# Performance work log

Measured on AMD Instinct MI355X. Metric: run time of the kernel, lower is better.

The kernel has to match this reference:

```python
import jax, jax.numpy as jnp
import numpy as np

B, SQ, SK, D, H = 4, 2048, 2048, 1024, 16
HD = D // H
LN_EPS = 1e-5


def setup_inputs() -> dict:
    key = jax.random.key(0)
    ks = jax.random.split(key, 16)
    s = 0.02
    return {
        "query": jax.random.normal(ks[0], (B, SQ, D), jnp.float32),
        "key": jax.random.normal(ks[1], (B, SK, D), jnp.float32),
        "value": jax.random.normal(ks[2], (B, SK, D), jnp.float32),
        "attention_mask": jax.random.randint(ks[3], (B, 1, 1, SK), 0, 2, jnp.int32),
        "relative_position_bias": jax.random.normal(ks[4], (1, H, SQ, SK), jnp.float32) * s,
        "Wq": jax.random.normal(ks[5], (D, D), jnp.float32) * s,
        "bq": jnp.zeros((D,), jnp.float32),
        "Wk": jax.random.normal(ks[6], (D, D), jnp.float32) * s,
        "bk": jnp.zeros((D,), jnp.float32),
        "Wv": jax.random.normal(ks[7], (D, D), jnp.float32) * s,
        "bv": jnp.zeros((D,), jnp.float32),
        "Wo": jax.random.normal(ks[8], (D, D), jnp.float32) * s,
        "bo": jnp.zeros((D,), jnp.float32),
        "ln_gamma": jnp.ones((D,), jnp.float32),
        "ln_beta": jnp.zeros((D,), jnp.float32),
    }


def reference(query, key, value, attention_mask, relative_position_bias,
              Wq, bq, Wk, bk, Wv, bv, Wo, bo, ln_gamma, ln_beta):
    # projections (torch Linear: x @ W.T + b)
    q = query @ Wq.T + bq   # [B,Sq,D]
    k = key @ Wk.T + bk     # [B,Sk,D]
    v = value @ Wv.T + bv   # [B,Sk,D]
    # split heads -> [B,H,S,hd]
    q = q.reshape(B, SQ, H, HD).transpose(0, 2, 1, 3)
    k = k.reshape(B, SK, H, HD).transpose(0, 2, 1, 3)
    v = v.reshape(B, SK, H, HD).transpose(0, 2, 1, 3)
    scores = jnp.einsum('bhqd,bhkd->bhqk', q, k) / jnp.sqrt(jnp.float32(HD))
    scores = scores + relative_position_bias
    scores = jnp.where(attention_mask == 0, -jnp.inf, scores)
    weights = jax.nn.softmax(scores, axis=-1)  # [B,H,Sq,Sk]
    ctx = jnp.einsum('bhqk,bhkd->bhqd', weights, v)
    ctx = ctx.transpose(0, 2, 1, 3).reshape(B, SQ, D)
    out = ctx @ Wo.T + bo
    x = query + out
    mu = jnp.mean(x, axis=-1, keepdims=True)
    var = jnp.var(x, axis=-1, keepdims=True)
    return (x - mu) * jax.lax.rsqrt(var + LN_EPS) * ln_gamma + ln_beta
```

## Files before the change

### kernel.cpp

```cpp
#include <hip/hip_runtime.h>
#include <hip/hip_bf16.h>

#define B_   4
#define SQ_  2048
#define SK_  2048
#define D_   1024
#define H_   16
#define HD_  64

typedef __bf16 bf16_t;
typedef bf16_t bf16x8 __attribute__((ext_vector_type(8)));
typedef bf16_t bf16x4 __attribute__((ext_vector_type(4)));
typedef float  f32x4  __attribute__((ext_vector_type(4)));
typedef int    i32x4  __attribute__((ext_vector_type(4)));
typedef unsigned u32x2 __attribute__((ext_vector_type(2)));



__device__ __forceinline__ void gll16(const bf16_t* g, bf16_t* l) {
    __builtin_amdgcn_global_load_lds(
        (const __attribute__((address_space(1))) unsigned int*)g,
        (__attribute__((address_space(3))) unsigned int*)l, 16, 0, 0);
}

__global__ __launch_bounds__(256) void cvt_bf16(
    const float* __restrict__ p0, const float* __restrict__ p1,
    const float* __restrict__ p2, const float* __restrict__ p3,
    bf16_t* __restrict__ d, int n)
{
    int y = blockIdx.y;
    const float* s = (y == 0) ? p0 : (y == 1) ? p1 : (y == 2) ? p2 : p3;
    int i = (blockIdx.x * 256 + threadIdx.x) * 8;
    f32x4 a = *(const f32x4*)(s + i);
    f32x4 b = *(const f32x4*)(s + i + 4);
    bf16x8 o;
    #pragma unroll
    for (int j = 0; j < 4; j++) { o[j] = (bf16_t)a[j]; o[4 + j] = (bf16_t)b[j]; }
    *(bf16x8*)(d + (size_t)y * n + i) = o;
}

__global__ __launch_bounds__(256) void gemm_qkv(
    const bf16_t* __restrict__ xb,
    const bf16_t* __restrict__ wb,
    const float* __restrict__ bq, const float* __restrict__ bk, const float* __restrict__ bv,
    bf16_t* __restrict__ oq, bf16_t* __restrict__ ok, bf16_t* __restrict__ ov)
{
    __shared__ __align__(16) bf16_t lA[2][4096];
    __shared__ __align__(16) bf16_t lB[2][4096];

    int z = blockIdx.z;
    const bf16_t* A = xb + (size_t)z * 8192 * 1024;
    const bf16_t* Bm = wb + (size_t)z * 1024 * 1024;
    const float* bias = (z == 0) ? bq : (z == 1) ? bk : bv;
    bf16_t* out = (z == 0) ? oq : (z == 1) ? ok : ov;

    int tid = threadIdx.x;
    int w = tid >> 6, l = tid & 63, lr = l & 15, lg = l >> 4;
    int m0 = blockIdx.x * 128, n0 = blockIdx.y * 128;
    int wm = (w >> 1) * 64, wn = (w & 1) * 64;

    f32x4 zero4 = {0.f, 0.f, 0.f, 0.f};
    f32x4 acc[4][4];
    #pragma unroll
    for (int i = 0; i < 4; i++)
        #pragma unroll
        for (int j = 0; j < 4; j++) acc[i][j] = zero4;

    int s0 = tid, s1 = 256 + tid;
    int r0 = s0 >> 2, c0 = s0 & 3, r1 = s1 >> 2, c1 = s1 & 3;
    const bf16_t* a0 = A + (size_t)(m0 + r0) * 1024 + ((c0 ^ ((r0 >> 1) & 3)) * 8);
    const bf16_t* a1 = A + (size_t)(m0 + r1) * 1024 + ((c1 ^ ((r1 >> 1) & 3)) * 8);
    const bf16_t* b0 = Bm + (size_t)(n0 + r0) * 1024 + ((c0 ^ ((r0 >> 1) & 3)) * 8);
    const bf16_t* b1 = Bm + (size_t)(n0 + r1) * 1024 + ((c1 ^ ((r1 >> 1) & 3)) * 8);

    auto stage = [&](int buf, int kt) {
        gll16(a0 + kt * 32, &lA[buf][s0 * 8]);
        gll16(a1 + kt * 32, &lA[buf][s1 * 8]);
        gll16(b0 + kt * 32, &lB[buf][s0 * 8]);
        gll16(b1 + kt * 32, &lB[buf][s1 * 8]);
    };

    stage(0, 0);
    int buf = 0;
    #pragma unroll 1
    for (int kt = 0; kt < 32; ++kt) {
        __syncthreads();
        if (kt + 1 < 32) stage(buf ^ 1, kt + 1);
        bf16x8 af[4], bfr[4];
        #pragma unroll
        for (int i = 0; i < 4; i++) {
            int ra = wm + i * 16 + lr;
            af[i] = *(const bf16x8*)&lA[buf][ra * 32 + ((lg ^ ((ra >> 1) & 3)) * 8)];
            int rb = wn + i * 16 + lr;
            bfr[i] = *(const bf16x8*)&lB[buf][rb * 32 + ((lg ^ ((rb >> 1) & 3)) * 8)];
        }
        #pragma unroll
        for (int mi = 0; mi < 4; mi++)
            #pragma unroll
            for (int ni = 0; ni < 4; ni++)
                acc[mi][ni] = __builtin_amdgcn_mfma_f32_16x16x32_bf16(af[mi], bfr[ni], acc[mi][ni], 0, 0, 0);
        buf ^= 1;
    }

    #pragma unroll
    for (int mi = 0; mi < 4; mi++) {
        int row = m0 + wm + mi * 16 + lg * 4;
        int bb_ = row >> 11;
        int s   = row & 2047;
        #pragma unroll
        for (int ni = 0; ni < 4; ni++) {
            int col = n0 + wn + ni * 16 + lr;
            int hh = col >> 6, d6 = col & 63;
            float bval = bias[col];
            if (z == 0) {
                size_t obase = (((size_t)bb_ * H_ + hh) * SQ_ + s) * HD_ + d6;
                #pragma unroll
                for (int r = 0; r < 4; r++)
                    out[obase + (size_t)r * HD_] = (bf16_t)((acc[mi][ni][r] + bval) * 0.125f);
            } else if (z == 1) {
                int kt = s >> 6, kpb = s & 63;
                size_t tb = (((size_t)bb_ * H_ + hh) * 32 + kt) * 4096;
                #pragma unroll
                for (int r = 0; r < 4; r++) {
                    int kp = kpb + r;
                    out[tb + (size_t)kp * 64 + (((d6 >> 3) ^ (kp & 7)) * 8) + (d6 & 7)] =
                        (bf16_t)(acc[mi][ni][r] + bval);
                }
            } else {
                int kt = s >> 6, kpb = s & 63;
                int chunk = ((kpb >> 5) & 1) * 4 + ((kpb >> 2) & 3);
                int jb    = ((kpb >> 4) & 1) * 4;
                size_t tb = (((size_t)bb_ * H_ + hh) * 32 + kt) * 4096;
                bf16x4 o4;
                #pragma unroll
                for (int r = 0; r < 4; r++) o4[r] = (bf16_t)(acc[mi][ni][r] + bval);
                *(bf16x4*)(out + tb + (size_t)d6 * 64 + ((chunk ^ (d6 & 7)) * 8) + jb) = o4;
            }
        }
    }
}

__global__ __launch_bounds__(256) void gemm_out(
    const bf16_t* __restrict__ A, const bf16_t* __restrict__ Bm,
    const float* __restrict__ bias, const float* __restrict__ resid,
    float* __restrict__ out)
{
    __shared__ __align__(16) bf16_t lA[2][4096];
    __shared__ __align__(16) bf16_t lB[2][4096];

    int tid = threadIdx.x;
    int w = tid >> 6, l = tid & 63, lr = l & 15, lg = l >> 4;
    int m0 = blockIdx.x * 128, n0 = blockIdx.y * 128;
    int wm = (w >> 1) * 64, wn = (w & 1) * 64;

    f32x4 zero4 = {0.f, 0.f, 0.f, 0.f};
    f32x4 acc[4][4];
    #pragma unroll
    for (int i = 0; i < 4; i++)
        #pragma unroll
        for (int j = 0; j < 4; j++) acc[i][j] = zero4;

    int s0 = tid, s1 = 256 + tid;
    int r0 = s0 >> 2, c0 = s0 & 3, r1 = s1 >> 2, c1 = s1 & 3;
    const bf16_t* a0 = A + (size_t)(m0 + r0) * 1024 + ((c0 ^ ((r0 >> 1) & 3)) * 8);
    const bf16_t* a1 = A + (size_t)(m0 + r1) * 1024 + ((c1 ^ ((r1 >> 1) & 3)) * 8);
    const bf16_t* b0 = Bm + (size_t)(n0 + r0) * 1024 + ((c0 ^ ((r0 >> 1) & 3)) * 8);
    const bf16_t* b1 = Bm + (size_t)(n0 + r1) * 1024 + ((c1 ^ ((r1 >> 1) & 3)) * 8);

    auto stage = [&](int buf, int kt) {
        gll16(a0 + kt * 32, &lA[buf][s0 * 8]);
        gll16(a1 + kt * 32, &lA[buf][s1 * 8]);
        gll16(b0 + kt * 32, &lB[buf][s0 * 8]);
        gll16(b1 + kt * 32, &lB[buf][s1 * 8]);
    };

    stage(0, 0);
    int buf = 0;
    #pragma unroll 1
    for (int kt = 0; kt < 32; ++kt) {
        __syncthreads();
        if (kt + 1 < 32) stage(buf ^ 1, kt + 1);
        bf16x8 af[4], bfr[4];
        #pragma unroll
        for (int i = 0; i < 4; i++) {
            int ra = wm + i * 16 + lr;
            af[i] = *(const bf16x8*)&lA[buf][ra * 32 + ((lg ^ ((ra >> 1) & 3)) * 8)];
            int rb = wn + i * 16 + lr;
            bfr[i] = *(const bf16x8*)&lB[buf][rb * 32 + ((lg ^ ((rb >> 1) & 3)) * 8)];
        }
        #pragma unroll
        for (int mi = 0; mi < 4; mi++)
            #pragma unroll
            for (int ni = 0; ni < 4; ni++)
                acc[mi][ni] = __builtin_amdgcn_mfma_f32_16x16x32_bf16(af[mi], bfr[ni], acc[mi][ni], 0, 0, 0);
        buf ^= 1;
    }

    #pragma unroll
    for (int mi = 0; mi < 4; mi++) {
        int row = m0 + wm + mi * 16 + lg * 4;
        #pragma unroll
        for (int ni = 0; ni < 4; ni++) {
            int col = n0 + wn + ni * 16 + lr;
            float bval = bias[col];
            #pragma unroll
            for (int r = 0; r < 4; r++) {
                size_t o = (size_t)(row + r) * D_ + col;
                out[o] = acc[mi][ni][r] + bval + resid[o];
            }
        }
    }
}

__global__ __launch_bounds__(256, 3) void attn_kernel(
    const bf16_t* __restrict__ qg, const bf16_t* __restrict__ kgt,
    const bf16_t* __restrict__ vgt, const float* __restrict__ bias,
    const int* __restrict__ mask, bf16_t* __restrict__ ctx)
{
    __shared__ __align__(16) bf16_t ksh[2][4096];
    __shared__ __align__(16) bf16_t vsh[2][4096];
    __shared__ __align__(8) unsigned char mlds[256];

    int x = blockIdx.x;
    int g8 = x & 7;
    int rest = x >> 3;
    int b  = rest & 3;
    int tt = ((rest >> 2) << 3) | g8;
    int h  = tt >> 4;
    int qt = tt & 15;

    int tid = threadIdx.x;
    int w   = tid >> 6;
    int l   = tid & 63;
    int q16 = l & 15;
    int g   = l >> 4;
    int g4  = g * 4;

    int qrow0 = qt * 128 + w * 16 + q16;
    int qrow1 = qrow0 + 64;
    const bf16_t* qbase = qg + ((size_t)b * H_ + h) * SQ_ * HD_;
    bf16x8 qf00 = *(const bf16x8*)(qbase + (size_t)qrow0 * HD_ + g * 8);
    bf16x8 qf01 = *(const bf16x8*)(qbase + (size_t)qrow0 * HD_ + 32 + g * 8);
    bf16x8 qf10 = *(const bf16x8*)(qbase + (size_t)qrow1 * HD_ + g * 8);
    bf16x8 qf11 = *(const bf16x8*)(qbase + (size_t)qrow1 * HD_ + 32 + g * 8);

    const bf16_t* kt_base = kgt + ((size_t)b * H_ + h) * 32 * 4096;
    const bf16_t* vt_base = vgt + ((size_t)b * H_ + h) * 32 * 4096;
    const float* bias_row0 = bias + ((size_t)h * SQ_ + qrow0) * SK_;
    const float* bias_row1 = bias + ((size_t)h * SQ_ + qrow1) * SK_;

    f32x4 zero4 = {0.f, 0.f, 0.f, 0.f};
    f32x4 oacc0[4], oacc1[4];
    #pragma unroll
    for (int i = 0; i < 4; i++) { oacc0[i] = zero4; oacc1[i] = zero4; }
    float l_r0 = 0.f, l_r1 = 0.f;

    auto stage = [&](int buf, int t) {
        const bf16_t* ks = kt_base + (size_t)t * 4096 + tid * 8;
        const bf16_t* vs = vt_base + (size_t)t * 4096 + tid * 8;
        gll16(ks,        &ksh[buf][tid * 8]);
        gll16(ks + 2048, &ksh[buf][2048 + tid * 8]);
        gll16(vs,        &vsh[buf][tid * 8]);
        gll16(vs + 2048, &vsh[buf][2048 + tid * 8]);
    };

    auto body = [&](const bf16_t* kb, const bf16_t* vb, int t) {
        f32x4 bb0[4], bb1[4];
        const float* bp0 = bias_row0 + t * 64 + g4;
        const float* bp1 = bias_row1 + t * 64 + g4;
        #pragma unroll
        for (int ni = 0; ni < 4; ni++) {
            bb0[ni] = *(const f32x4*)(bp0 + ni * 16);
            bb1[ni] = *(const f32x4*)(bp1 + ni * 16);
        }
        u32x2 mm = *(const u32x2*)&mlds[t * 8];
        unsigned lo = mm[0], hi = mm[1];

        f32x4 s0[4], s1[4];
        __builtin_amdgcn_s_setprio(1);
        #pragma unroll
        for (int ni = 0; ni < 4; ni++) {
            int krow = ni * 16 + q16;
            const bf16_t* kr = kb + krow * 64;
            bf16x8 kf0 = *(const bf16x8*)(kr + ((g       ^ (krow & 7)) * 8));
            bf16x8 kf1 = *(const bf16x8*)(kr + (((4 + g) ^ (krow & 7)) * 8));
            s0[ni] = zero4; s1[ni] = zero4;
            s0[ni] = __builtin_amdgcn_mfma_f32_16x16x32_bf16(kf0, qf00, s0[ni], 0, 0, 0);
            s0[ni] = __builtin_amdgcn_mfma_f32_16x16x32_bf16(kf1, qf01, s0[ni], 0, 0, 0);
            s1[ni] = __builtin_amdgcn_mfma_f32_16x16x32_bf16(kf0, qf10, s1[ni], 0, 0, 0);
            s1[ni] = __builtin_amdgcn_mfma_f32_16x16x32_bf16(kf1, qf11, s1[ni], 0, 0, 0);
        }
        __builtin_amdgcn_s_setprio(0);

        unsigned n0_ = (lo >> g4) & 0xF;
        unsigned n1_ = (lo >> (16 + g4)) & 0xF;
        unsigned n2_ = (hi >> g4) & 0xF;
        unsigned n3_ = (hi >> (16 + g4)) & 0xF;

        float rs0 = 0.f, rs1 = 0.f;
        bf16x8 pA0, pA1, pB0, pB1;
        #pragma unroll
        for (int r = 0; r < 4; r++) {
            float e0 = __expf(s0[0][r] + bb0[0][r]); e0 = ((n0_ >> r) & 1) ? e0 : 0.f;
            float e1 = __expf(s0[1][r] + bb0[1][r]); e1 = ((n1_ >> r) & 1) ? e1 : 0.f;
            float e2 = __expf(s0[2][r] + bb0[2][r]); e2 = ((n2_ >> r) & 1) ? e2 : 0.f;
            float e3 = __expf(s0[3][r] + bb0[3][r]); e3 = ((n3_ >> r) & 1) ? e3 : 0.f;
            rs0 += (e0 + e1) + (e2 + e3);
            pA0[r] = (bf16_t)e0; pA0[4 + r] = (bf16_t)e1;
            pA1[r] = (bf16_t)e2; pA1[4 + r] = (bf16_t)e3;
            float f0 = __expf(s1[0][r] + bb1[0][r]); f0 = ((n0_ >> r) & 1) ? f0 : 0.f;
            float f1 = __expf(s1[1][r] + bb1[1][r]); f1 = ((n1_ >> r) & 1) ? f1 : 0.f;
            float f2 = __expf(s1[2][r] + bb1[2][r]); f2 = ((n2_ >> r) & 1) ? f2 : 0.f;
            float f3 = __expf(s1[3][r] + bb1[3][r]); f3 = ((n3_ >> r) & 1) ? f3 : 0.f;
            rs1 += (f0 + f1) + (f2 + f3);
            pB0[r] = (bf16_t)f0; pB0[4 + r] = (bf16_t)f1;
            pB1[r] = (bf16_t)f2; pB1[4 + r] = (bf16_t)f3;
        }
        l_r0 += rs0; l_r1 += rs1;

        __builtin_amdgcn_s_setprio(1);
        #pragma unroll
        for (int nd = 0; nd < 4; nd++) {
            int vrow = nd * 16 + q16;
            const bf16_t* vr = vb + vrow * 64;
            bf16x8 vf0 = *(const bf16x8*)(vr + ((g       ^ (vrow & 7)) * 8));
            bf16x8 vf1 = *(const bf16x8*)(vr + (((4 + g) ^ (vrow & 7)) * 8));
            oacc0[nd] = __builtin_amdgcn_mfma_f32_16x16x32_bf16(vf0, pA0, oacc0[nd], 0, 0, 0);
            oacc0[nd] = __builtin_amdgcn_mfma_f32_16x16x32_bf16(vf1, pA1, oacc0[nd], 0, 0, 0);
            oacc1[nd] = __builtin_amdgcn_mfma_f32_16x16x32_bf16(vf0, pB0, oacc1[nd], 0, 0, 0);
            oacc1[nd] = __builtin_amdgcn_mfma_f32_16x16x32_bf16(vf1, pB1, oacc1[nd], 0, 0, 0);
        }
        __builtin_amdgcn_s_setprio(0);
    };

    stage(0, 0);
    stage(1, 1);
    {
        const int* mp = mask + (size_t)b * SK_ + tid * 8;
        i32x4 u0 = *(const i32x4*)mp;
        i32x4 u1 = *(const i32x4*)(mp + 4);
        unsigned by = 0;
        #pragma unroll
        for (int j = 0; j < 4; j++) by |= (u0[j] != 0 ? 1u : 0u) << j;
        #pragma unroll
        for (int j = 0; j < 4; j++) by |= (u1[j] != 0 ? 1u : 0u) << (4 + j);
        mlds[tid] = (unsigned char)by;
    }
    __syncthreads();

    #pragma unroll 1
    for (int t = 0; t < 32; ++t) {
        int buf = t & 1;
        if (t) {
            asm volatile("s_waitcnt vmcnt(4)" ::: "memory");
            __builtin_amdgcn_s_barrier();
            __builtin_amdgcn_sched_barrier(0);
        }
        body(ksh[buf], vsh[buf], t);
        asm volatile("" ::: "memory");
        __builtin_amdgcn_s_barrier();
        __builtin_amdgcn_sched_barrier(0);
        if (t + 2 < 32) stage(buf, t + 2);
    }

    l_r0 += __shfl_xor(l_r0, 16);
    l_r0 += __shfl_xor(l_r0, 32);
    l_r1 += __shfl_xor(l_r1, 16);
    l_r1 += __shfl_xor(l_r1, 32);
    float inv0 = (l_r0 > 0.f) ? 1.0f / l_r0 : 0.f;
    float inv1 = (l_r1 > 0.f) ? 1.0f / l_r1 : 0.f;

    bf16_t* cp0 = ctx + ((size_t)b * SQ_ + qrow0) * D_ + (size_t)h * HD_;
    bf16_t* cp1 = ctx + ((size_t)b * SQ_ + qrow1) * D_ + (size_t)h * HD_;
    #pragma unroll
    for (int nd = 0; nd < 4; nd++) {
        bf16x4 o4, o5;
        #pragma unroll
        for (int r = 0; r < 4; r++) {
            o4[r] = (bf16_t)(oacc0[nd][r] * inv0);
            o5[r] = (bf16_t)(oacc1[nd][r] * inv1);
        }
        *(bf16x4*)(cp0 + nd * 16 + g4) = o4;
        *(bf16x4*)(cp1 + nd * 16 + g4) = o5;
    }
}

__global__ __launch_bounds__(256) void ln_kernel(
    const float* __restrict__ x, const float* __restrict__ gamma,
    const float* __restrict__ beta, float* __restrict__ out)
{
    int row = blockIdx.x;
    int t = threadIdx.x;
    const float* src = x + (size_t)row * D_;
    f32x4 v = *(const f32x4*)(src + t * 4);
    float s  = v[0] + v[1] + v[2] + v[3];
    float s2 = v[0] * v[0] + v[1] * v[1] + v[2] * v[2] + v[3] * v[3];
    #pragma unroll
    for (int off = 32; off > 0; off >>= 1) {
        s  += __shfl_down(s, off);
        s2 += __shfl_down(s2, off);
    }
    __shared__ float red[8];
    int w = t >> 6, l = t & 63;
    if (l == 0) { red[w] = s; red[4 + w] = s2; }
    __syncthreads();
    if (t == 0) {
        red[0] = red[0] + red[1] + red[2] + red[3];
        red[4] = red[4] + red[5] + red[6] + red[7];
    }
    __syncthreads();
    float mu  = red[0] * (1.0f / D_);
    float var = red[4] * (1.0f / D_) - mu * mu;
    float rstd = rsqrtf(var + 1e-5f);
    f32x4 g  = *(const f32x4*)(gamma + t * 4);
    f32x4 be = *(const f32x4*)(beta + t * 4);
    f32x4 o;
    #pragma unroll
    for (int i = 0; i < 4; i++) o[i] = (v[i] - mu) * rstd * g[i] + be[i];
    *(f32x4*)(out + (size_t)row * D_ + t * 4) = o;
}

extern "C" void kernel_launch(void* const* d_in, const int* in_sizes, int n_in,
                              void* d_out, int out_size, void* d_ws, size_t ws_size,
                              hipStream_t stream)
{
    const float* query = (const float*)d_in[0];
    const float* key   = (const float*)d_in[1];
    const float* value = (const float*)d_in[2];
    const int*   mask  = (const int*)d_in[3];
    const float* bias  = (const float*)d_in[4];
    const float* Wq    = (const float*)d_in[5];
    const float* bq    = (const float*)d_in[6];
    const float* Wk    = (const float*)d_in[7];
    const float* bk    = (const float*)d_in[8];
    const float* Wv    = (const float*)d_in[9];
    const float* bv    = (const float*)d_in[10];
    const float* Wo    = (const float*)d_in[11];
    const float* bo    = (const float*)d_in[12];
    const float* gamma = (const float*)d_in[13];
    const float* beta  = (const float*)d_in[14];
    float* out = (float*)d_out;

    char* ws = (char*)d_ws;
    const size_t MB = 1024 * 1024;
    bf16_t* xb  = (bf16_t*)(ws);
    bf16_t* ctx = (bf16_t*)(ws);
    float*  tmp = (float*)(ws + 16 * MB);
    bf16_t* wb  = (bf16_t*)(ws + 48 * MB);
    bf16_t* qb  = (bf16_t*)(ws + 56 * MB);
    bf16_t* kgt = (bf16_t*)(ws + 72 * MB);
    bf16_t* vgt = (bf16_t*)(ws + 88 * MB);

    cvt_bf16<<<dim3(4096, 3), 256, 0, stream>>>(query, key, value, query, xb, 8192 * 1024);
    cvt_bf16<<<dim3(512, 4), 256, 0, stream>>>(Wq, Wk, Wv, Wo, wb, 1024 * 1024);
    gemm_qkv<<<dim3(64, 8, 3), 256, 0, stream>>>(xb, wb, bq, bk, bv, qb, kgt, vgt);
    attn_kernel<<<dim3(1024), 256, 0, stream>>>(qb, kgt, vgt, bias, mask, ctx);
    gemm_out<<<dim3(64, 8), 256, 0, stream>>>(ctx, wb + (size_t)3 * 1024 * 1024, bo, query, tmp);
    ln_kernel<<<dim3(8192), 256, 0, stream>>>(tmp, gamma, beta, out);
}
```

Measured before the change: 329.1 us.

## Prefetch attention bias one tile ahead with inline asm loads and raise occupancy

Bias loads for the next key tile are now issued through inline-asm global_load_dwordx4 in the middle of the current iteration, so their latency overlaps the PV MFMAs and the next QK MFMAs instead of stalling before the exponentials. The waitcnt values are rewritten by hand to track the extra outstanding loads, and the mask loading is moved ahead of the staging. Launch bounds also go from 3 to 4 blocks per CU, which caps register use. This adds register pressure from keeping the bias across iterations, risks spills under the tighter bound, and relies on vmcnt counting being exactly right.

```diff
diff --git a/kernel.cpp b/kernel.cpp
--- a/kernel.cpp
+++ b/kernel.cpp
@@ -22,6 +22,9 @@
         (const __attribute__((address_space(1))) unsigned int*)g,
         (__attribute__((address_space(3))) unsigned int*)l, 16, 0, 0);
 }
+
+#define GLOAD4_OFF(dst, ptr, OFFSTR) \
+    asm volatile("global_load_dwordx4 %0, %1, off" OFFSTR : "=&v"(dst) : "v"(ptr))
 
 __global__ __launch_bounds__(256) void cvt_bf16(
     const float* __restrict__ p0, const float* __restrict__ p1,
@@ -212,7 +215,7 @@
     }
 }
 
-__global__ __launch_bounds__(256, 3) void attn_kernel(
+__global__ __launch_bounds__(256, 4) void attn_kernel(
     const bf16_t* __restrict__ qg, const bf16_t* __restrict__ kgt,
     const bf16_t* __restrict__ vgt, const float* __restrict__ bias,
     const int* __restrict__ mask, bf16_t* __restrict__ ctx)
@@ -246,8 +249,8 @@
 
     const bf16_t* kt_base = kgt + ((size_t)b * H_ + h) * 32 * 4096;
     const bf16_t* vt_base = vgt + ((size_t)b * H_ + h) * 32 * 4096;
-    const float* bias_row0 = bias + ((size_t)h * SQ_ + qrow0) * SK_;
-    const float* bias_row1 = bias + ((size_t)h * SQ_ + qrow1) * SK_;
+    const float* bp0 = bias + ((size_t)h * SQ_ + qrow0) * SK_ + g4;
+    const float* bp1 = bias + ((size_t)h * SQ_ + qrow1) * SK_ + g4;
 
     f32x4 zero4 = {0.f, 0.f, 0.f, 0.f};
     f32x4 oacc0[4], oacc1[4];
@@ -264,15 +267,45 @@
         gll16(vs + 2048, &vsh[buf][2048 + tid * 8]);
     };
 
-    auto body = [&](const bf16_t* kb, const bf16_t* vb, int t) {
-        f32x4 bb0[4], bb1[4];
-        const float* bp0 = bias_row0 + t * 64 + g4;
-        const float* bp1 = bias_row1 + t * 64 + g4;
-        #pragma unroll
-        for (int ni = 0; ni < 4; ni++) {
-            bb0[ni] = *(const f32x4*)(bp0 + ni * 16);
-            bb1[ni] = *(const f32x4*)(bp1 + ni * 16);
-        }
+    f32x4 bb0[4], bb1[4];
+    auto bias_issue = [&]() {
+        GLOAD4_OFF(bb0[0], bp0, "");
+        GLOAD4_OFF(bb0[1], bp0, " offset:64");
+        GLOAD4_OFF(bb0[2], bp0, " offset:128");
+        GLOAD4_OFF(bb0[3], bp0, " offset:192");
+        GLOAD4_OFF(bb1[0], bp1, "");
+        GLOAD4_OFF(bb1[1], bp1, " offset:64");
+        GLOAD4_OFF(bb1[2], bp1, " offset:128");
+        GLOAD4_OFF(bb1[3], bp1, " offset:192");
+        bp0 += 64; bp1 += 64;
+    };
+
+    {
+        const int* mp = mask + (size_t)b * SK_ + tid * 8;
+        i32x4 u0 = *(const i32x4*)mp;
+        i32x4 u1 = *(const i32x4*)(mp + 4);
+        unsigned by = 0;
+        #pragma unroll
+        for (int j = 0; j < 4; j++) by |= (u0[j] != 0 ? 1u : 0u) << j;
+        #pragma unroll
+        for (int j = 0; j < 4; j++) by |= (u1[j] != 0 ? 1u : 0u) << (4 + j);
+        mlds[tid] = (unsigned char)by;
+    }
+    stage(0, 0);
+    stage(1, 1);
+    bias_issue();
+    __syncthreads();
+
+    #pragma unroll 1
+    for (int t = 0; t < 32; ++t) {
+        int buf = t & 1;
+        if (t > 0) {
+            if (t == 31) asm volatile("s_waitcnt vmcnt(8)" ::: "memory");
+            else         asm volatile("s_waitcnt vmcnt(12)" ::: "memory");
+            __builtin_amdgcn_s_barrier();
+            __builtin_amdgcn_sched_barrier(0);
+        }
+
         u32x2 mm = *(const u32x2*)&mlds[t * 8];
         unsigned lo = mm[0], hi = mm[1];
 
@@ -281,7 +314,7 @@
         #pragma unroll
         for (int ni = 0; ni < 4; ni++) {
             int krow = ni * 16 + q16;
-            const bf16_t* kr = kb + krow * 64;
+            const bf16_t* kr = &ksh[buf][0] + krow * 64;
             bf16x8 kf0 = *(const bf16x8*)(kr + ((g       ^ (krow & 7)) * 8));
             bf16x8 kf1 = *(const bf16x8*)(kr + (((4 + g) ^ (krow & 7)) * 8));
             s0[ni] = zero4; s1[ni] = zero4;
@@ -291,6 +324,10 @@
             s1[ni] = __builtin_amdgcn_mfma_f32_16x16x32_bf16(kf1, qf11, s1[ni], 0, 0, 0);
         }
         __builtin_amdgcn_s_setprio(0);
+
+        if (t == 31) asm volatile("s_waitcnt vmcnt(0)" ::: "memory");
+        else         asm volatile("s_waitcnt vmcnt(4)" ::: "memory");
+        __builtin_amdgcn_sched_barrier(0);
 
         unsigned n0_ = (lo >> g4) & 0xF;
         unsigned n1_ = (lo >> (16 + g4)) & 0xF;
@@ -317,12 +354,15 @@
             pB1[r] = (bf16_t)f2; pB1[4 + r] = (bf16_t)f3;
         }
         l_r0 += rs0; l_r1 += rs1;
+        __builtin_amdgcn_sched_barrier(0);
+
+        if (t < 31) bias_issue();
 
         __builtin_amdgcn_s_setprio(1);
         #pragma unroll
         for (int nd = 0; nd < 4; nd++) {
             int vrow = nd * 16 + q16;
-            const bf16_t* vr = vb + vrow * 64;
+            const bf16_t* vr = &vsh[buf][0] + vrow * 64;
             bf16x8 vf0 = *(const bf16x8*)(vr + ((g       ^ (vrow & 7)) * 8));
             bf16x8 vf1 = *(const bf16x8*)(vr + (((4 + g) ^ (vrow & 7)) * 8));
             oacc0[nd] = __builtin_amdgcn_mfma_f32_16x16x32_bf16(vf0, pA0, oacc0[nd], 0, 0, 0);
@@ -331,32 +371,7 @@
             oacc1[nd] = __builtin_amdgcn_mfma_f32_16x16x32_bf16(vf1, pB1, oacc1[nd], 0, 0, 0);
         }
         __builtin_amdgcn_s_setprio(0);
-    };
-
-    stage(0, 0);
-    stage(1, 1);
-    {
-        const int* mp = mask + (size_t)b * SK_ + tid * 8;
-        i32x4 u0 = *(const i32x4*)mp;
-        i32x4 u1 = *(const i32x4*)(mp + 4);
-        unsigned by = 0;
-        #pragma unroll
-        for (int j = 0; j < 4; j++) by |= (u0[j] != 0 ? 1u : 0u) << j;
-        #pragma unroll
-        for (int j = 0; j < 4; j++) by |= (u1[j] != 0 ? 1u : 0u) << (4 + j);
-        mlds[tid] = (unsigned char)by;
-    }
-    __syncthreads();
-
-    #pragma unroll 1
-    for (int t = 0; t < 32; ++t) {
-        int buf = t & 1;
-        if (t) {
-            asm volatile("s_waitcnt vmcnt(4)" ::: "memory");
-            __builtin_amdgcn_s_barrier();
-            __builtin_amdgcn_sched_barrier(0);
-        }
-        body(ksh[buf], vsh[buf], t);
+
         asm volatile("" ::: "memory");
         __builtin_amdgcn_s_barrier();
         __builtin_amdgcn_sched_barrier(0);
```

Result: slower. 745.6 us (+126.6%).
